# Optimization experiments

Hardware: AMD Instinct MI355X
Metric: run time of the kernel (lower is better)

Reference implementation:

```python
import jax, jax.numpy as jnp
import numpy as np

D_MODEL = 1024
D_HEAD = 64
NHEADS = 8
IN_DIM = D_HEAD * NHEADS  # 512
EPS = 1e-5

def layernorm(x, g, b):
    mu = jnp.mean(x, axis=-1, keepdims=True)
    var = jnp.var(x, axis=-1, keepdims=True)
    return (x - mu) * jax.lax.rsqrt(var + EPS) * g + b

def setup_inputs() -> dict:
    key = jax.random.key(0)
    ks = jax.random.split(key, 8)
    B, M, L = 4, 8192, 64
    x = jax.random.normal(ks[0], (B, M, D_MODEL), dtype=jnp.float32)
    latents = jax.random.normal(ks[1], (B, L, D_MODEL), dtype=jnp.float32)
    s = 1.0 / np.sqrt(D_MODEL)
    Wq = jax.random.normal(ks[2], (D_MODEL, IN_DIM), dtype=jnp.float32) * s
    Wkv = jax.random.normal(ks[3], (D_MODEL, 2 * IN_DIM), dtype=jnp.float32) * s
    Wout = jax.random.normal(ks[4], (IN_DIM, D_MODEL), dtype=jnp.float32) * (1.0 / np.sqrt(IN_DIM))
    gm = jnp.ones((D_MODEL,), jnp.float32); bm = jnp.zeros((D_MODEL,), jnp.float32)
    gl = jnp.ones((D_MODEL,), jnp.float32); bl = jnp.zeros((D_MODEL,), jnp.float32)
    return {"x": x, "latents": latents, "Wq": Wq, "Wkv": Wkv, "Wout": Wout,
            "gm": gm, "bm": bm, "gl": gl, "bl": bl}

def reference(x, latents, Wq, Wkv, Wout, gm, bm, gl, bl):
    scale = D_HEAD ** (-0.5)
    xn = layernorm(x, gm, bm)            # [B, M, D]
    ln = layernorm(latents, gl, bl)      # [B, L, D]
    q = ln @ Wq                          # [B, L, IN_DIM]
    kv_input = jnp.concatenate([xn, ln], axis=-2)   # [B, M+L, D]
    kv = kv_input @ Wkv                  # [B, M+L, 2*IN_DIM]
    k, v = jnp.split(kv, 2, axis=-1)
    def heads(t):
        B, S, _ = t.shape
        return t.reshape(B, S, NHEADS, D_HEAD).transpose(0, 2, 1, 3)  # [B,H,S,dh]
    q, k, v = heads(q), heads(k), heads(v)
    q = q / scale  # NOTE: original divides by d_head**-0.5 (i.e. multiplies by sqrt(d_head))
    sim = jnp.einsum('bhid,bhjd->bhij', q, k)         # [B,H,L,M+L]
    sim = sim - jax.lax.stop_gradient(jnp.max(sim, axis=-1, keepdims=True))
    attn = jax.nn.softmax(sim, axis=-1)
    out = jnp.einsum('bhij,bhjd->bhid', attn, v)      # [B,H,L,dh]
    B, H, L, dh = out.shape
    out = out.transpose(0, 2, 1, 3).reshape(B, L, H * dh)
    return out @ Wout                                 # [B, L, D]
```

## Files before the change

### kernel.cpp

```cpp
#include <hip/hip_runtime.h>
#include <math.h>

#define DM 1024
#define INDIM 512
#define NH 8
#define DH 64
#define LQ 64
#define BATCH 4
#define MX 8192
#define SKV 8256
#define MROWS (BATCH * SKV)

typedef _Float16 f16;
typedef f16 f16x8 __attribute__((ext_vector_type(8)));
typedef f16 f16x4 __attribute__((ext_vector_type(4)));
typedef float f32x4 __attribute__((ext_vector_type(4)));

__global__ __launch_bounds__(256) void ln_kernel(const float* __restrict__ src,
        const float* __restrict__ gam, const float* __restrict__ bet,
        f16* __restrict__ dst, f16* __restrict__ dst2,
        int rpb_in, int dst_off)
{
    int r = blockIdx.x;
    int tid = threadIdx.x;
    int b = r / rpb_in, m = r % rpb_in;
    const float4 v = *(const float4*)(src + (size_t)r * DM + tid * 4);
    float s = v.x + v.y + v.z + v.w;
    float q = v.x * v.x + v.y * v.y + v.z * v.z + v.w * v.w;
    for (int off = 32; off; off >>= 1) { s += __shfl_xor(s, off); q += __shfl_xor(q, off); }
    __shared__ float ps[4], pq[4];
    int w = tid >> 6;
    if ((tid & 63) == 0) { ps[w] = s; pq[w] = q; }
    __syncthreads();
    s = ps[0] + ps[1] + ps[2] + ps[3];
    q = pq[0] + pq[1] + pq[2] + pq[3];
    float mean = s * (1.f / DM);
    float var = q * (1.f / DM) - mean * mean;
    float rstd = rsqrtf(var + 1e-5f);
    const float4 gg = *(const float4*)(gam + tid * 4);
    const float4 bb = *(const float4*)(bet + tid * 4);
    f16x4 o;
    o[0] = (f16)((v.x - mean) * rstd * gg.x + bb.x);
    o[1] = (f16)((v.y - mean) * rstd * gg.y + bb.y);
    o[2] = (f16)((v.z - mean) * rstd * gg.z + bb.z);
    o[3] = (f16)((v.w - mean) * rstd * gg.w + bb.w);
    size_t drow = (size_t)b * SKV + dst_off + m;
    *(f16x4*)(dst + drow * DM + tid * 4) = o;
    if (dst2) *(f16x4*)(dst2 + (size_t)r * DM + tid * 4) = o;
}

__global__ __launch_bounds__(256) void transpose_w(const float* __restrict__ src,
        f16* __restrict__ dst, int R, int C, float scale)
{
    __shared__ float tile[32][33];
    int c0 = blockIdx.x * 32, r0 = blockIdx.y * 32;
    int tx = threadIdx.x & 31;
    int ty = threadIdx.x >> 5;
    #pragma unroll
    for (int k = 0; k < 4; k++)
        tile[ty + k * 8][tx] = src[(size_t)(r0 + ty + k * 8) * C + c0 + tx];
    __syncthreads();
    #pragma unroll
    for (int k = 0; k < 4; k++)
        dst[(size_t)(c0 + ty + k * 8) * R + r0 + tx] = (f16)(tile[tx][ty + k * 8] * scale);
}

template<int MODE>
__global__ __launch_bounds__(256) void gemm_bt(const f16* __restrict__ A, const f16* __restrict__ Bt,
        f16* __restrict__ Chi, f16* __restrict__ Clo,
        float* __restrict__ Cf, f16* __restrict__ vT,
        int M, int N, int K)
{
    __shared__ f16 As[128 * 40];
    __shared__ f16 Bs[128 * 40];
    int tid = threadIdx.x;
    int w = tid >> 6, l = tid & 63, l15 = l & 15, gq = l >> 4;
    int wr = w >> 1, wc = w & 1;
    int bm = blockIdx.x, bn = blockIdx.y;
    const f16* Ap = A + (size_t)(bm * 128 + (tid >> 1)) * K + (tid & 1) * 16;
    const f16* Bp = Bt + (size_t)(bn * 128 + (tid >> 1)) * K + (tid & 1) * 16;
    f16* As_w = &As[(tid >> 1) * 40 + (tid & 1) * 16];
    f16* Bs_w = &Bs[(tid >> 1) * 40 + (tid & 1) * 16];
    f32x4 acc[4][4] = {};
    for (int k0 = 0; k0 < K; k0 += 32) {
        f16x8 a0 = *(const f16x8*)(Ap + k0);
        f16x8 a1 = *(const f16x8*)(Ap + k0 + 8);
        f16x8 b0 = *(const f16x8*)(Bp + k0);
        f16x8 b1 = *(const f16x8*)(Bp + k0 + 8);
        __syncthreads();
        *(f16x8*)As_w = a0; *(f16x8*)(As_w + 8) = a1;
        *(f16x8*)Bs_w = b0; *(f16x8*)(Bs_w + 8) = b1;
        __syncthreads();
        f16x8 af[4], bfr[4];
        #pragma unroll
        for (int mm = 0; mm < 4; mm++)
            af[mm] = *(const f16x8*)&As[(wr * 64 + mm * 16 + l15) * 40 + gq * 8];
        #pragma unroll
        for (int nn = 0; nn < 4; nn++)
            bfr[nn] = *(const f16x8*)&Bs[(wc * 64 + nn * 16 + l15) * 40 + gq * 8];
        #pragma unroll
        for (int mm = 0; mm < 4; mm++)
            #pragma unroll
            for (int nn = 0; nn < 4; nn++)
                acc[mm][nn] = __builtin_amdgcn_mfma_f32_16x16x32_f16(af[mm], bfr[nn], acc[mm][nn], 0, 0, 0);
    }
    int rowb = bm * 128 + wr * 64 + gq * 4;
    int colb = bn * 128 + wc * 64 + l15;
    #pragma unroll
    for (int mm = 0; mm < 4; mm++)
    #pragma unroll
    for (int nn = 0; nn < 4; nn++)
    #pragma unroll
    for (int i = 0; i < 4; i++) {
        int row = rowb + mm * 16 + i;
        int col = colb + nn * 16;
        float v = acc[mm][nn][i];
        if (MODE == 1) {
            Cf[(size_t)row * N + col] = v;
        } else if (MODE == 3) {
            f16 hi = (f16)v;
            Chi[(size_t)row * N + col] = hi;
            Clo[(size_t)row * N + col] = (f16)(v - (float)hi);
        } else {
            if (col < INDIM) {
                f16 hi = (f16)v;
                Chi[(size_t)row * INDIM + col] = hi;
                Clo[(size_t)row * INDIM + col] = (f16)(v - (float)hi);
            } else {
                int b = row / SKV; int key = row - b * SKV;
                int hd = col - INDIM;
                vT[(size_t)((b * NH + (hd >> 6)) * DH + (hd & 63)) * SKV + key] = (f16)v;
            }
        }
    }
}

__global__ __launch_bounds__(512) void attn_kernel(const f16* __restrict__ q_hi, const f16* __restrict__ q_lo,
        const f16* __restrict__ k_hi, const f16* __restrict__ k_lo,
        const f16* __restrict__ vT, f16* __restrict__ attn_out)
{
    __shared__ f16 P_lds[8][64][40];
    __shared__ float O_sum[64][64];
    __shared__ float m_lds[8][64];
    __shared__ float l_lds[8][64];
    int bh = blockIdx.x; int b = bh >> 3, h = bh & 7;
    int tid = threadIdx.x, w = tid >> 6, l = tid & 63, l15 = l & 15, gq = l >> 4;
    for (int i = tid; i < 64 * 64; i += 512) ((float*)O_sum)[i] = 0.f;
    f16x8 qfh[4][2], qfl[4][2];
    #pragma unroll
    for (int nb = 0; nb < 4; nb++)
        #pragma unroll
        for (int dh = 0; dh < 2; dh++) {
            size_t off = (size_t)(b * LQ + nb * 16 + l15) * INDIM + h * DH + dh * 32 + gq * 8;
            qfh[nb][dh] = *(const f16x8*)&q_hi[off];
            qfl[nb][dh] = *(const f16x8*)&q_lo[off];
        }
    const f16* kbh = k_hi + (size_t)b * SKV * INDIM + h * DH;
    const f16* kbl = k_lo + (size_t)b * SKV * INDIM + h * DH;
    const f16* vb = vT + (size_t)bh * DH * SKV;
    f32x4 accO[4][4] = {};
    float m_st[4] = {-1e30f, -1e30f, -1e30f, -1e30f};
    float l_st[4] = {0.f, 0.f, 0.f, 0.f};
    __syncthreads();
    for (int t = w; t < 258; t += 8) {
        int key0 = t * 32;
        f32x4 S[2][4] = {};
        f16x8 kah[2][2], kal[2][2];
        #pragma unroll
        for (int kbi = 0; kbi < 2; kbi++)
            #pragma unroll
            for (int dh = 0; dh < 2; dh++) {
                size_t off = (size_t)(key0 + kbi * 16 + l15) * INDIM + dh * 32 + gq * 8;
                kah[kbi][dh] = *(const f16x8*)&kbh[off];
                kal[kbi][dh] = *(const f16x8*)&kbl[off];
            }
        #pragma unroll
        for (int kbi = 0; kbi < 2; kbi++)
            #pragma unroll
            for (int nb = 0; nb < 4; nb++) {
                S[kbi][nb] = __builtin_amdgcn_mfma_f32_16x16x32_f16(kah[kbi][0], qfh[nb][0], S[kbi][nb], 0, 0, 0);
                S[kbi][nb] = __builtin_amdgcn_mfma_f32_16x16x32_f16(kah[kbi][1], qfh[nb][1], S[kbi][nb], 0, 0, 0);
                S[kbi][nb] = __builtin_amdgcn_mfma_f32_16x16x32_f16(kah[kbi][0], qfl[nb][0], S[kbi][nb], 0, 0, 0);
                S[kbi][nb] = __builtin_amdgcn_mfma_f32_16x16x32_f16(kah[kbi][1], qfl[nb][1], S[kbi][nb], 0, 0, 0);
                S[kbi][nb] = __builtin_amdgcn_mfma_f32_16x16x32_f16(kal[kbi][0], qfh[nb][0], S[kbi][nb], 0, 0, 0);
                S[kbi][nb] = __builtin_amdgcn_mfma_f32_16x16x32_f16(kal[kbi][1], qfh[nb][1], S[kbi][nb], 0, 0, 0);
            }
        #pragma unroll
        for (int nb = 0; nb < 4; nb++) {
            float tm = -1e30f;
            #pragma unroll
            for (int kbi = 0; kbi < 2; kbi++)
                #pragma unroll
                for (int i = 0; i < 4; i++) tm = fmaxf(tm, S[kbi][nb][i]);
            tm = fmaxf(tm, __shfl_xor(tm, 16));
            tm = fmaxf(tm, __shfl_xor(tm, 32));
            float nm = fmaxf(m_st[nb], tm);
            float corr = __expf(m_st[nb] - nm);
            m_st[nb] = nm;
            float rs = 0.f;
            #pragma unroll
            for (int kbi = 0; kbi < 2; kbi++) {
                f16x4 pk;
                #pragma unroll
                for (int i = 0; i < 4; i++) {
                    float p = __expf(S[kbi][nb][i] - nm);
                    rs += p;
                    pk[i] = (f16)p;
                }
                *(f16x4*)&P_lds[w][nb * 16 + l15][kbi * 16 + gq * 4] = pk;
            }
            rs += __shfl_xor(rs, 16);
            rs += __shfl_xor(rs, 32);
            l_st[nb] = l_st[nb] * corr + rs;
            #pragma unroll
            for (int db = 0; db < 4; db++) accO[db][nb] *= corr;
        }
        #pragma unroll
        for (int db = 0; db < 4; db++) {
            f16x8 va = *(const f16x8*)&vb[(size_t)(db * 16 + l15) * SKV + key0 + gq * 8];
            #pragma unroll
            for (int nb = 0; nb < 4; nb++) {
                f16x8 pb = *(const f16x8*)&P_lds[w][nb * 16 + l15][gq * 8];
                accO[db][nb] = __builtin_amdgcn_mfma_f32_16x16x32_f16(va, pb, accO[db][nb], 0, 0, 0);
            }
        }
    }
    if (gq == 0) {
        #pragma unroll
        for (int nb = 0; nb < 4; nb++) {
            m_lds[w][nb * 16 + l15] = m_st[nb];
            l_lds[w][nb * 16 + l15] = l_st[nb];
        }
    }
    __syncthreads();
    #pragma unroll
    for (int nb = 0; nb < 4; nb++) {
        int qrow = nb * 16 + l15;
        float Mx = -1e30f;
        #pragma unroll
        for (int ww = 0; ww < 8; ww++) Mx = fmaxf(Mx, m_lds[ww][qrow]);
        float f = __expf(m_st[nb] - Mx);
        #pragma unroll
        for (int db = 0; db < 4; db++)
            #pragma unroll
            for (int i = 0; i < 4; i++)
                atomicAdd(&O_sum[db * 16 + gq * 4 + i][qrow], accO[db][nb][i] * f);
    }
    __syncthreads();
    {
        int qrow = tid >> 3, d0 = (tid & 7) * 8;
        float Mx = -1e30f;
        #pragma unroll
        for (int ww = 0; ww < 8; ww++) Mx = fmaxf(Mx, m_lds[ww][qrow]);
        float Ls = 0.f;
        #pragma unroll
        for (int ww = 0; ww < 8; ww++) Ls += l_lds[ww][qrow] * __expf(m_lds[ww][qrow] - Mx);
        float inv = 1.f / Ls;
        f16x8 o;
        #pragma unroll
        for (int j = 0; j < 8; j++) o[j] = (f16)(O_sum[d0 + j][qrow] * inv);
        *(f16x8*)&attn_out[(size_t)(b * LQ + qrow) * INDIM + h * DH + d0] = o;
    }
}

extern "C" void kernel_launch(void* const* d_in, const int* in_sizes, int n_in,
                              void* d_out, int out_size, void* d_ws, size_t ws_size,
                              hipStream_t stream)
{
    const float* x    = (const float*)d_in[0];
    const float* lat  = (const float*)d_in[1];
    const float* Wq   = (const float*)d_in[2];
    const float* Wkv  = (const float*)d_in[3];
    const float* Wout = (const float*)d_in[4];
    const float* gm   = (const float*)d_in[5];
    const float* bm   = (const float*)d_in[6];
    const float* gl   = (const float*)d_in[7];
    const float* bl   = (const float*)d_in[8];
    float* out = (float*)d_out;

    char* ws = (char*)d_ws;
    size_t off = 0;
    auto alloc = [&](size_t bytes) {
        char* p = ws + off;
        off += (bytes + 255) & ~(size_t)255;
        return p;
    };
    f16* kv_in  = (f16*)alloc((size_t)MROWS * DM * 2);
    f16* k_hi   = (f16*)alloc((size_t)MROWS * INDIM * 2);
    f16* k_lo   = (f16*)alloc((size_t)MROWS * INDIM * 2);
    f16* vT     = (f16*)alloc((size_t)BATCH * NH * DH * SKV * 2);
    f16* q_in   = (f16*)alloc((size_t)BATCH * LQ * DM * 2);
    f16* q_hi   = (f16*)alloc((size_t)BATCH * LQ * INDIM * 2);
    f16* q_lo   = (f16*)alloc((size_t)BATCH * LQ * INDIM * 2);
    f16* wq_t   = (f16*)alloc((size_t)INDIM * DM * 2);
    f16* wkv_t  = (f16*)alloc((size_t)DM * DM * 2);
    f16* wout_t = (f16*)alloc((size_t)DM * INDIM * 2);
    f16* attn_o = (f16*)alloc((size_t)BATCH * LQ * INDIM * 2);

    transpose_w<<<dim3(INDIM / 32, DM / 32), 256, 0, stream>>>(Wq, wq_t, DM, INDIM, 8.0f);
    transpose_w<<<dim3(DM / 32, DM / 32), 256, 0, stream>>>(Wkv, wkv_t, DM, DM, 1.0f);
    transpose_w<<<dim3(DM / 32, INDIM / 32), 256, 0, stream>>>(Wout, wout_t, INDIM, DM, 1.0f);
    ln_kernel<<<BATCH * MX, 256, 0, stream>>>(x, gm, bm, kv_in, nullptr, MX, 0);
    ln_kernel<<<BATCH * LQ, 256, 0, stream>>>(lat, gl, bl, kv_in, q_in, LQ, MX);
    gemm_bt<3><<<dim3(2, INDIM / 128), 256, 0, stream>>>(q_in, wq_t, q_hi, q_lo, nullptr, nullptr,
                                                         BATCH * LQ, INDIM, DM);
    gemm_bt<2><<<dim3(MROWS / 128, DM / 128), 256, 0, stream>>>(kv_in, wkv_t, k_hi, k_lo, nullptr, vT,
                                                                MROWS, DM, DM);
    attn_kernel<<<BATCH * NH, 512, 0, stream>>>(q_hi, q_lo, k_hi, k_lo, vT, attn_o);
    gemm_bt<1><<<dim3(2, DM / 128), 256, 0, stream>>>(attn_o, wout_t, nullptr, nullptr, out, nullptr,
                                                      BATCH * LQ, DM, INDIM);
}
```

Baseline: 547.6 us.

## Split attention over key chunks with merge kernel; load GEMM tiles directly to LDS

The attention kernel now splits the key sequence into 8 chunks, so it launches 256 blocks instead of 32 and can occupy far more CUs. Each block writes its unnormalized partial output plus the running max and sum to scratch that reuses the kv_in buffer. A new merge kernel combines the chunks with log-sum-exp rescaling and normalizes the result. Separately, the KV/Q/out GEMM now stages A and B tiles with global_load_lds into unpadded LDS, skipping the register round-trip; the cost is possible LDS bank conflicts on the fragment reads.

```diff
diff --git a/kernel.cpp b/kernel.cpp
--- a/kernel.cpp
+++ b/kernel.cpp
@@ -10,11 +10,21 @@
 #define MX 8192
 #define SKV 8256
 #define MROWS (BATCH * SKV)
+#define NBH (BATCH * NH)
+#define NT 258
+#define NCHUNK 8
+#define TPC 33
 
 typedef _Float16 f16;
 typedef f16 f16x8 __attribute__((ext_vector_type(8)));
 typedef f16 f16x4 __attribute__((ext_vector_type(4)));
 typedef float f32x4 __attribute__((ext_vector_type(4)));
+
+typedef __attribute__((address_space(1))) const unsigned int gu32;
+typedef __attribute__((address_space(3))) unsigned int lu32;
+__device__ __forceinline__ void gload16(const f16* g, f16* l) {
+    __builtin_amdgcn_global_load_lds((gu32*)g, (lu32*)l, 16, 0, 0);
+}
 
 __global__ __launch_bounds__(256) void ln_kernel(const float* __restrict__ src,
         const float* __restrict__ gam, const float* __restrict__ bet,
@@ -71,33 +81,34 @@
         float* __restrict__ Cf, f16* __restrict__ vT,
         int M, int N, int K)
 {
-    __shared__ f16 As[128 * 40];
-    __shared__ f16 Bs[128 * 40];
+    __shared__ f16 As[128 * 32];
+    __shared__ f16 Bs[128 * 32];
     int tid = threadIdx.x;
     int w = tid >> 6, l = tid & 63, l15 = l & 15, gq = l >> 4;
     int wr = w >> 1, wc = w & 1;
     int bm = blockIdx.x, bn = blockIdx.y;
-    const f16* Ap = A + (size_t)(bm * 128 + (tid >> 1)) * K + (tid & 1) * 16;
-    const f16* Bp = Bt + (size_t)(bn * 128 + (tid >> 1)) * K + (tid & 1) * 16;
-    f16* As_w = &As[(tid >> 1) * 40 + (tid & 1) * 16];
-    f16* Bs_w = &Bs[(tid >> 1) * 40 + (tid & 1) * 16];
+    const f16* gA = A + (size_t)(bm * 128 + w * 32 + (l >> 2)) * K + (l & 3) * 8;
+    const f16* gB = Bt + (size_t)(bn * 128 + w * 32 + (l >> 2)) * K + (l & 3) * 8;
+    f16* lA0 = As + w * 1024;
+    f16* lA1 = As + w * 1024 + 512;
+    f16* lB0 = Bs + w * 1024;
+    f16* lB1 = Bs + w * 1024 + 512;
+    const size_t j1 = (size_t)16 * K;
     f32x4 acc[4][4] = {};
     for (int k0 = 0; k0 < K; k0 += 32) {
-        f16x8 a0 = *(const f16x8*)(Ap + k0);
-        f16x8 a1 = *(const f16x8*)(Ap + k0 + 8);
-        f16x8 b0 = *(const f16x8*)(Bp + k0);
-        f16x8 b1 = *(const f16x8*)(Bp + k0 + 8);
         __syncthreads();
-        *(f16x8*)As_w = a0; *(f16x8*)(As_w + 8) = a1;
-        *(f16x8*)Bs_w = b0; *(f16x8*)(Bs_w + 8) = b1;
+        gload16(gA + k0, lA0);
+        gload16(gA + k0 + j1, lA1);
+        gload16(gB + k0, lB0);
+        gload16(gB + k0 + j1, lB1);
         __syncthreads();
         f16x8 af[4], bfr[4];
         #pragma unroll
         for (int mm = 0; mm < 4; mm++)
-            af[mm] = *(const f16x8*)&As[(wr * 64 + mm * 16 + l15) * 40 + gq * 8];
+            af[mm] = *(const f16x8*)&As[(wr * 64 + mm * 16 + l15) * 32 + gq * 8];
         #pragma unroll
         for (int nn = 0; nn < 4; nn++)
-            bfr[nn] = *(const f16x8*)&Bs[(wc * 64 + nn * 16 + l15) * 40 + gq * 8];
+            bfr[nn] = *(const f16x8*)&Bs[(wc * 64 + nn * 16 + l15) * 32 + gq * 8];
         #pragma unroll
         for (int mm = 0; mm < 4; mm++)
             #pragma unroll
@@ -137,13 +148,18 @@
 
 __global__ __launch_bounds__(512) void attn_kernel(const f16* __restrict__ q_hi, const f16* __restrict__ q_lo,
         const f16* __restrict__ k_hi, const f16* __restrict__ k_lo,
-        const f16* __restrict__ vT, f16* __restrict__ attn_out)
+        const f16* __restrict__ vT,
+        float* __restrict__ pO, float* __restrict__ pm, float* __restrict__ pl)
 {
     __shared__ f16 P_lds[8][64][40];
     __shared__ float O_sum[64][64];
     __shared__ float m_lds[8][64];
     __shared__ float l_lds[8][64];
-    int bh = blockIdx.x; int b = bh >> 3, h = bh & 7;
+    int bh = blockIdx.x & (NBH - 1);
+    int chunk = blockIdx.x >> 5;
+    int b = bh >> 3, h = bh & 7;
+    int cstart = chunk * TPC;
+    int cend = cstart + TPC; if (cend > NT) cend = NT;
     int tid = threadIdx.x, w = tid >> 6, l = tid & 63, l15 = l & 15, gq = l >> 4;
     for (int i = tid; i < 64 * 64; i += 512) ((float*)O_sum)[i] = 0.f;
     f16x8 qfh[4][2], qfl[4][2];
@@ -162,7 +178,7 @@
     float m_st[4] = {-1e30f, -1e30f, -1e30f, -1e30f};
     float l_st[4] = {0.f, 0.f, 0.f, 0.f};
     __syncthreads();
-    for (int t = w; t < 258; t += 8) {
+    for (int t = cstart + w; t < cend; t += 8) {
         int key0 = t * 32;
         f32x4 S[2][4] = {};
         f16x8 kah[2][2], kal[2][2];
@@ -255,12 +271,60 @@
         float Ls = 0.f;
         #pragma unroll
         for (int ww = 0; ww < 8; ww++) Ls += l_lds[ww][qrow] * __expf(m_lds[ww][qrow] - Mx);
-        float inv = 1.f / Ls;
-        f16x8 o;
-        #pragma unroll
-        for (int j = 0; j < 8; j++) o[j] = (f16)(O_sum[d0 + j][qrow] * inv);
-        *(f16x8*)&attn_out[(size_t)(b * LQ + qrow) * INDIM + h * DH + d0] = o;
-    }
+        size_t base = ((size_t)(bh * NCHUNK + chunk) * 64 + qrow) * 64 + d0;
+        float4 o0, o1;
+        o0.x = O_sum[d0 + 0][qrow]; o0.y = O_sum[d0 + 1][qrow];
+        o0.z = O_sum[d0 + 2][qrow]; o0.w = O_sum[d0 + 3][qrow];
+        o1.x = O_sum[d0 + 4][qrow]; o1.y = O_sum[d0 + 5][qrow];
+        o1.z = O_sum[d0 + 6][qrow]; o1.w = O_sum[d0 + 7][qrow];
+        *(float4*)&pO[base] = o0;
+        *(float4*)&pO[base + 4] = o1;
+        if (d0 == 0) {
+            pm[(bh * NCHUNK + chunk) * 64 + qrow] = Mx;
+            pl[(bh * NCHUNK + chunk) * 64 + qrow] = Ls;
+        }
+    }
+}
+
+__global__ __launch_bounds__(256) void attn_merge(const float* __restrict__ pO,
+        const float* __restrict__ pm, const float* __restrict__ pl, f16* __restrict__ attn_out)
+{
+    int bh = blockIdx.x; int b = bh >> 3, h = bh & 7;
+    int tid = threadIdx.x;
+    int row = tid >> 2, dseg = tid & 3;
+    float pmv[NCHUNK];
+    float mx = -1e30f;
+    #pragma unroll
+    for (int c = 0; c < NCHUNK; c++) {
+        pmv[c] = pm[(bh * NCHUNK + c) * 64 + row];
+        mx = fmaxf(mx, pmv[c]);
+    }
+    float L = 0.f;
+    float wgt[NCHUNK];
+    #pragma unroll
+    for (int c = 0; c < NCHUNK; c++) {
+        wgt[c] = __expf(pmv[c] - mx);
+        L += pl[(bh * NCHUNK + c) * 64 + row] * wgt[c];
+    }
+    float inv = 1.f / L;
+    float acc[16] = {};
+    #pragma unroll
+    for (int c = 0; c < NCHUNK; c++) {
+        const float* p = &pO[((size_t)(bh * NCHUNK + c) * 64 + row) * 64 + dseg * 16];
+        float wc = wgt[c];
+        #pragma unroll
+        for (int jj = 0; jj < 4; jj++) {
+            float4 a = *(const float4*)(p + jj * 4);
+            acc[jj * 4 + 0] += a.x * wc; acc[jj * 4 + 1] += a.y * wc;
+            acc[jj * 4 + 2] += a.z * wc; acc[jj * 4 + 3] += a.w * wc;
+        }
+    }
+    f16 o[16];
+    #pragma unroll
+    for (int j = 0; j < 16; j++) o[j] = (f16)(acc[j] * inv);
+    f16* dst = &attn_out[(size_t)(b * LQ + row) * INDIM + h * DH + dseg * 16];
+    *(f16x8*)dst = *(f16x8*)&o[0];
+    *(f16x8*)(dst + 8) = *(f16x8*)&o[8];
 }
 
 extern "C" void kernel_launch(void* const* d_in, const int* in_sizes, int n_in,
@@ -296,6 +360,9 @@
     f16* wkv_t  = (f16*)alloc((size_t)DM * DM * 2);
     f16* wout_t = (f16*)alloc((size_t)DM * INDIM * 2);
     f16* attn_o = (f16*)alloc((size_t)BATCH * LQ * INDIM * 2);
+    float* pO   = (float*)kv_in;
+    float* pm   = (float*)((char*)kv_in + (size_t)NBH * NCHUNK * 64 * 64 * 4);
+    float* pl   = (float*)((char*)pm + (size_t)NBH * NCHUNK * 64 * 4);
 
     transpose_w<<<dim3(INDIM / 32, DM / 32), 256, 0, stream>>>(Wq, wq_t, DM, INDIM, 8.0f);
     transpose_w<<<dim3(DM / 32, DM / 32), 256, 0, stream>>>(Wkv, wkv_t, DM, DM, 1.0f);
@@ -306,7 +373,8 @@
                                                          BATCH * LQ, INDIM, DM);
     gemm_bt<2><<<dim3(MROWS / 128, DM / 128), 256, 0, stream>>>(kv_in, wkv_t, k_hi, k_lo, nullptr, vT,
                                                                 MROWS, DM, DM);
-    attn_kernel<<<BATCH * NH, 512, 0, stream>>>(q_hi, q_lo, k_hi, k_lo, vT, attn_o);
+    attn_kernel<<<NBH * NCHUNK, 512, 0, stream>>>(q_hi, q_lo, k_hi, k_lo, vT, pO, pm, pl);
+    attn_merge<<<NBH, 256, 0, stream>>>(pO, pm, pl, attn_o);
     gemm_bt<1><<<dim3(2, DM / 128), 256, 0, stream>>>(attn_o, wout_t, nullptr, nullptr, out, nullptr,
                                                       BATCH * LQ, DM, INDIM);
 }
```

Measured after the change: 477.0 us. 1.15x faster.
